# Kernel tuning notes

Hardware: AMD Instinct MI355X
Metric: run time of the kernel (lower is better)

## Reference

```python
import jax, jax.numpy as jnp
import numpy as np

B, N, H = 32, 2048, 256          # batch, num_docs, hidden_dim
F_HEADS = 8                      # config.dynamic_fusion_heads
NH = 8                           # num_heads inside each nn.MultiheadAttention
STEPS = 3                        # config.meta_adaptation_steps


def setup_inputs() -> dict:
    key = jax.random.key(0)
    ks = jax.random.split(key, 10)
    s = 0.02
    return {
        "query": jax.random.normal(ks[0], (B, H), jnp.float32),
        "retrieved_docs": jax.random.normal(ks[1], (B, N, H), jnp.float32),
        "causal_weights": jax.random.uniform(ks[2], (B, N, 1), jnp.float32),
        "context_history": jax.random.normal(ks[3], (B, H), jnp.float32),
        # per-fusion-head MultiheadAttention params (torch layout: in_proj [3H,H])
        "in_proj_w": jax.random.normal(ks[4], (F_HEADS, 3 * H, H), jnp.float32) * s,
        "in_proj_b": jnp.zeros((F_HEADS, 3 * H), jnp.float32),
        "out_proj_w": jax.random.normal(ks[5], (F_HEADS, H, H), jnp.float32) * s,
        "out_proj_b": jnp.zeros((F_HEADS, H), jnp.float32),
        "strategy_w": jax.random.normal(ks[6], (F_HEADS, H), jnp.float32) * s,
        "strategy_b": jnp.zeros((F_HEADS,), jnp.float32),
        "meta_params": jax.random.normal(ks[7], (STEPS, H, H), jnp.float32) * 0.02,
    }


def _mha_qlen1(q, kv, Wi, bi, Wo, bo):
    # q: [B,H] (query length 1), kv: [B,N,H]. Torch MHA semantics, batch_first.
    Wq, Wk, Wv = jnp.split(Wi, 3, axis=0)
    bq, bk, bv = jnp.split(bi, 3)
    dh = H // NH
    qh = (q @ Wq.T + bq).reshape(B, NH, dh)
    kh = (kv @ Wk.T + bk).reshape(B, N, NH, dh)
    vh = (kv @ Wv.T + bv).reshape(B, N, NH, dh)
    scores = jnp.einsum('bhd,bnhd->bhn', qh, kh) / jnp.sqrt(jnp.float32(dh))
    attn = jax.nn.softmax(scores, axis=-1)
    ctx = jnp.einsum('bhn,bnhd->bhd', attn, vh).reshape(B, H)
    return ctx @ Wo.T + bo


def reference(query, retrieved_docs, causal_weights, context_history,
              in_proj_w, in_proj_b, out_proj_w, out_proj_b,
              strategy_w, strategy_b, meta_params):
    # causal weighting of retrieved docs (shared across all fusion heads)
    weighted_docs = retrieved_docs * causal_weights  # [B,N,H]

    # batch all 8 fusion heads' cross-attention in one vmapped pass -> [F,B,H]
    heads_out = jax.vmap(
        lambda Wi, bi, Wo, bo: _mha_qlen1(query, weighted_docs, Wi, bi, Wo, bo)
    )(in_proj_w, in_proj_b, out_proj_w, out_proj_b)

    # sequential residual meta-adaptation steps (same matrices for every head)
    for i in range(STEPS):
        heads_out = heads_out + heads_out @ meta_params[i]

    # strategy-weighted combine of fusion heads
    strategy = jax.nn.softmax(query @ strategy_w.T + strategy_b, axis=-1)  # [B,F]
    return jnp.einsum('fbh,bf->bh', heads_out, strategy)  # [B,H]
```

## Files before the change

### kernel.cpp

```cpp
#include <hip/hip_runtime.h>
#include <hip/hip_bf16.h>


#define B_ 32
#define N_ 2048
#define H_ 256
#define F_ 8
#define FH_ 64
#define NCH_ 8

typedef unsigned short u16;
typedef __attribute__((ext_vector_type(8))) short bf16x8;
typedef __attribute__((ext_vector_type(4))) float f32x4;
#define MFMA(a, b, c) __builtin_amdgcn_mfma_f32_16x16x32_bf16((a), (b), (c), 0, 0, 0)

__device__ __forceinline__ u16 f2b(float x) {
  unsigned u = __builtin_bit_cast(unsigned, x);
  return (u16)((u + 0x7fffu + ((u >> 16) & 1u)) >> 16);
}
__device__ __forceinline__ float b2f(u16 h) {
  unsigned u = ((unsigned)h) << 16;
  return __builtin_bit_cast(float, u);
}
__device__ __forceinline__ bf16x8 ld8b(const float* p) {
  float4 v0 = *(const float4*)p, v1 = *(const float4*)(p + 4);
  bf16x8 a;
  a[0] = f2b(v0.x); a[1] = f2b(v0.y); a[2] = f2b(v0.z); a[3] = f2b(v0.w);
  a[4] = f2b(v1.x); a[5] = f2b(v1.y); a[6] = f2b(v1.z); a[7] = f2b(v1.w);
  return a;
}

static constexpr size_t UB_U     = 0;
static constexpr size_t UB_W     = 1048576;
static constexpr size_t UB_L     = 3145728;
static constexpr size_t UB_STRAT = 3153920;
static constexpr size_t UB_MT    = 3154944;

__global__ __launch_bounds__(512) void k1_fused(
    const float* __restrict__ query, const float* __restrict__ ipw,
    const float* __restrict__ ipb, const float* __restrict__ stw,
    const float* __restrict__ stb, const float* __restrict__ meta,
    u16* __restrict__ u, u16* __restrict__ metaT, float* __restrict__ strat)
{
  const int tid = threadIdx.x, L = tid & 63, w = tid >> 6;
  const int khi = L >> 4, col = L & 15;

  if (blockIdx.x >= 16) {
    const int bid2 = blockIdx.x - 16;
    const int s = bid2 >> 3, x0 = (bid2 & 7) * 32;
    __shared__ u16 sT[32 * 264];
    #pragma unroll
    for (int p = 0; p < 4; ++p) {
      int idx = tid + 512 * p;
      int r = idx >> 3, xq = (idx & 7) * 4;
      float4 v = *(const float4*)&meta[((size_t)(s * 256) + r) * 256 + x0 + xq];
      sT[(xq + 0) * 264 + r] = f2b(v.x);
      sT[(xq + 1) * 264 + r] = f2b(v.y);
      sT[(xq + 2) * 264 + r] = f2b(v.z);
      sT[(xq + 3) * 264 + r] = f2b(v.w);
    }
    __syncthreads();
    #pragma unroll
    for (int p = 0; p < 2; ++p) {
      int idx = tid + 512 * p;
      int x = idx >> 5, rq = (idx & 31) * 8;
      bf16x8 v = *(bf16x8*)&sT[x * 264 + rq];
      *(bf16x8*)&metaT[((size_t)(s * 256) + x0 + x) * 256 + rq] = v;
    }
    return;
  }

  const int f = blockIdx.x >> 1, hf = blockIdx.x & 1;
  __shared__ u16 sW[256 * 40];
  __shared__ u16 qhh[32 * 136];
  __shared__ u16 qhl[32 * 136];
  __shared__ float slog[256];

  bf16x8 qf[2][8];
  #pragma unroll
  for (int bt = 0; bt < 2; ++bt)
    #pragma unroll
    for (int ks = 0; ks < 8; ++ks)
      qf[bt][ks] = ld8b(&query[(size_t)(bt * 16 + col) * H_ + ks * 32 + khi * 8]);

  if (f == 0 && hf == 0 && w == 0) {
    f32x4 sacc[2] = {(f32x4){0.f,0.f,0.f,0.f}, (f32x4){0.f,0.f,0.f,0.f}};
    #pragma unroll
    for (int ks = 0; ks < 8; ++ks) {
      bf16x8 a = (bf16x8){0,0,0,0,0,0,0,0};
      if (col < 8) a = ld8b(&stw[(size_t)col * H_ + ks * 32 + khi * 8]);
      sacc[0] = MFMA(a, qf[0][ks], sacc[0]);
      sacc[1] = MFMA(a, qf[1][ks], sacc[1]);
    }
    if (khi < 2) {
      #pragma unroll
      for (int bt = 0; bt < 2; ++bt)
        #pragma unroll
        for (int r = 0; r < 4; ++r) {
          int i = khi * 4 + r;
          slog[(bt * 16 + col) * 8 + i] = sacc[bt][r] + stb[i];
        }
    }
  }

  f32x4 qacc[2] = {(f32x4){0.f,0.f,0.f,0.f}, (f32x4){0.f,0.f,0.f,0.f}};
  for (int ks = 0; ks < 8; ++ks) {
    #pragma unroll
    for (int p = 0; p < 2; ++p) {
      int gid = tid + 512 * p;
      int r = gid >> 3, kq = (gid & 7) * 4;
      float4 v = *(const float4*)&ipw[((size_t)(f * 768) + hf * 128 + r) * H_ + ks * 32 + kq];
      *(ushort4*)&sW[r * 40 + kq] = make_ushort4(f2b(v.x), f2b(v.y), f2b(v.z), f2b(v.w));
    }
    __syncthreads();
    bf16x8 a = *(const bf16x8*)&sW[(w * 16 + col) * 40 + khi * 8];
    qacc[0] = MFMA(a, qf[0][ks], qacc[0]);
    qacc[1] = MFMA(a, qf[1][ks], qacc[1]);
    __syncthreads();
  }
  {
    int r0 = w * 16 + khi * 4;
    float4 bq = *(const float4*)&ipb[f * 768 + hf * 128 + r0];
    #pragma unroll
    for (int bt = 0; bt < 2; ++bt) {
      int b = bt * 16 + col;
      float v0 = qacc[bt][0] + bq.x, v1 = qacc[bt][1] + bq.y;
      float v2 = qacc[bt][2] + bq.z, v3 = qacc[bt][3] + bq.w;
      ushort4 hs = make_ushort4(f2b(v0), f2b(v1), f2b(v2), f2b(v3));
      ushort4 ls = make_ushort4(f2b(v0 - b2f(hs.x)), f2b(v1 - b2f(hs.y)),
                                f2b(v2 - b2f(hs.z)), f2b(v3 - b2f(hs.w)));
      *(ushort4*)&qhh[b * 136 + r0] = hs;
      *(ushort4*)&qhl[b * 136 + r0] = ls;
    }
  }
  __syncthreads();

  if (f == 0 && hf == 0 && tid < 32) {
    float mx = slog[tid * 8];
    #pragma unroll
    for (int i = 1; i < F_; ++i) mx = fmaxf(mx, slog[tid * 8 + i]);
    float s = 0.f, e[F_];
    #pragma unroll
    for (int i = 0; i < F_; ++i) { e[i] = __expf(slog[tid * 8 + i] - mx); s += e[i]; }
    #pragma unroll
    for (int i = 0; i < F_; ++i) strat[tid * F_ + i] = e[i] / s;
  }

  const float scale = 0.17677669529663687f;
  for (int hh = 0; hh < 4; ++hh) {
    #pragma unroll
    for (int p = 0; p < 4; ++p) {
      int gid = tid + 512 * p;
      int d = gid >> 6, jq = (gid & 63) * 4;
      float4 v = *(const float4*)&ipw[((size_t)(f * 768 + 256) + (hf * 4 + hh) * 32 + d) * H_ + jq];
      float vv[4] = {v.x, v.y, v.z, v.w};
      #pragma unroll
      for (int e = 0; e < 4; ++e) {
        int j = jq + e;
        sW[j * 40 + (d ^ (((j >> 4) & 3) << 3))] = f2b(vv[e]);
      }
    }
    __syncthreads();
    #pragma unroll
    for (int q = 0; q < 2; ++q) {
      int jt = w * 2 + q;
      bf16x8 a = *(const bf16x8*)&sW[(jt * 16 + col) * 40 + ((khi ^ (jt & 3)) * 8)];
      #pragma unroll
      for (int bt = 0; bt < 2; ++bt) {
        int b = bt * 16 + col;
        bf16x8 bh = *(const bf16x8*)&qhh[b * 136 + hh * 32 + khi * 8];
        bf16x8 bl = *(const bf16x8*)&qhl[b * 136 + hh * 32 + khi * 8];
        f32x4 acc = (f32x4){0.f, 0.f, 0.f, 0.f};
        acc = MFMA(a, bh, acc);
        acc = MFMA(a, bl, acc);
        int j0 = jt * 16 + khi * 4;
        ushort4 us = make_ushort4(f2b(acc[0] * scale), f2b(acc[1] * scale),
                                  f2b(acc[2] * scale), f2b(acc[3] * scale));
        *(ushort4*)&u[((size_t)(b * 64) + f * 8 + hf * 4 + hh) * H_ + j0] = us;
      }
    }
    __syncthreads();
  }
}

__global__ __launch_bounds__(512) void k4_one(
    const float* __restrict__ docs, const float* __restrict__ cw,
    const u16* __restrict__ u, float* __restrict__ wbuf, float* __restrict__ lbuf)
{
  const int ns = blockIdx.x, b = blockIdx.y;
  const int n0 = ns * 256;
  const int tid = threadIdx.x, L = tid & 63, w = tid >> 6;
  const int khi = L >> 4, col = L & 15;
  const int ft = w & 3, nt0 = (w >> 2) * 2;

  __shared__ u16 sdu[64 * 264];
  __shared__ u16 phu[64 * 72];
  __shared__ u16 plou[64 * 72];

  bf16x8 uf[8];
  #pragma unroll
  for (int ks = 0; ks < 8; ++ks)
    uf[ks] = *(const bf16x8*)&u[((size_t)(b * 64) + ft * 16 + col) * H_ + ks * 32 + khi * 8];

  float4 dv[8];
  #pragma unroll
  for (int p = 0; p < 8; ++p) {
    int idx = tid + 512 * p;
    int n = idx >> 6, jq = (idx & 63) * 4;
    dv[p] = *(const float4*)&docs[((size_t)(b * N_) + n0 + n) * H_ + jq];
  }
  #pragma unroll
  for (int p = 0; p < 8; ++p) {
    int idx = tid + 512 * p;
    int n = idx >> 6, jq = (idx & 63) * 4;
    *(ushort4*)&sdu[n * 264 + (jq ^ (((n >> 3) & 3) << 4))] =
        make_ushort4(f2b(dv[p].x), f2b(dv[p].y), f2b(dv[p].z), f2b(dv[p].w));
  }
  __syncthreads();

  f32x4 acc2[4][2];
  #pragma unroll
  for (int mt = 0; mt < 4; ++mt)
    #pragma unroll
    for (int jt = 0; jt < 2; ++jt) acc2[mt][jt] = (f32x4){0.f, 0.f, 0.f, 0.f};
  float eacc[4] = {0.f, 0.f, 0.f, 0.f};

  for (int nc = 0; nc < 4; ++nc) {
    if (nc < 3) {
      #pragma unroll
      for (int p = 0; p < 8; ++p) {
        int idx = tid + 512 * p;
        int n = idx >> 6, jq = (idx & 63) * 4;
        dv[p] = *(const float4*)&docs[((size_t)(b * N_) + n0 + (nc + 1) * 64 + n) * H_ + jq];
      }
    }
    f32x4 sc0 = (f32x4){0.f, 0.f, 0.f, 0.f}, sc1 = sc0;
    const int nr0 = nt0 * 16 + col, nr1 = (nt0 + 1) * 16 + col;
    const int sw0 = ((nr0 >> 3) & 3) << 4, sw1 = ((nr1 >> 3) & 3) << 4;
    #pragma unroll
    for (int ks = 0; ks < 8; ++ks) {
      bf16x8 b0 = *(const bf16x8*)&sdu[nr0 * 264 + ((ks * 32 + khi * 8) ^ sw0)];
      bf16x8 b1 = *(const bf16x8*)&sdu[nr1 * 264 + ((ks * 32 + khi * 8) ^ sw1)];
      sc0 = MFMA(uf[ks], b0, sc0);
      sc1 = MFMA(uf[ks], b1, sc1);
    }
    {
      int ng = n0 + nc * 64 + nt0 * 16 + col;
      float cv0 = cw[(size_t)b * N_ + ng];
      float cv1 = cw[(size_t)b * N_ + ng + 16];
      #pragma unroll
      for (int r = 0; r < 4; ++r) {
        int fh = ft * 16 + khi * 4 + r;
        float ex0 = __expf(sc0[r] * cv0);
        float ex1 = __expf(sc1[r] * cv1);
        eacc[r] += ex0 + ex1;
        float p0 = ex0 * cv0, p1 = ex1 * cv1;
        u16 h0 = f2b(p0), h1 = f2b(p1);
        phu [fh * 72 + nt0 * 16 + col]       = h0;
        plou[fh * 72 + nt0 * 16 + col]       = f2b(p0 - b2f(h0));
        phu [fh * 72 + (nt0 + 1) * 16 + col] = h1;
        plou[fh * 72 + (nt0 + 1) * 16 + col] = f2b(p1 - b2f(h1));
      }
    }
    __syncthreads();

    #pragma unroll
    for (int kk = 0; kk < 2; ++kk) {
      #pragma unroll
      for (int jt = 0; jt < 2; ++jt) {
        int j = w * 32 + jt * 16 + col;
        bf16x8 bb;
        #pragma unroll
        for (int jj = 0; jj < 8; ++jj)
          bb[jj] = (short)sdu[(kk * 32 + khi * 8 + jj) * 264 + (j ^ (khi << 4))];
        #pragma unroll
        for (int mt = 0; mt < 4; ++mt) {
          bf16x8 ah = *(const bf16x8*)&phu [(mt * 16 + col) * 72 + kk * 32 + khi * 8];
          bf16x8 al = *(const bf16x8*)&plou[(mt * 16 + col) * 72 + kk * 32 + khi * 8];
          acc2[mt][jt] = MFMA(ah, bb, acc2[mt][jt]);
          acc2[mt][jt] = MFMA(al, bb, acc2[mt][jt]);
        }
      }
    }
    __syncthreads();

    if (nc < 3) {
      #pragma unroll
      for (int p = 0; p < 8; ++p) {
        int idx = tid + 512 * p;
        int n = idx >> 6, jq = (idx & 63) * 4;
        *(ushort4*)&sdu[n * 264 + (jq ^ (((n >> 3) & 3) << 4))] =
            make_ushort4(f2b(dv[p].x), f2b(dv[p].y), f2b(dv[p].z), f2b(dv[p].w));
      }
      __syncthreads();
    }
  }
  #pragma unroll
  for (int mt = 0; mt < 4; ++mt)
    #pragma unroll
    for (int jt = 0; jt < 2; ++jt)
      #pragma unroll
      for (int r = 0; r < 4; ++r) {
        int fh = mt * 16 + khi * 4 + r;
        int j = w * 32 + jt * 16 + col;
        atomicAdd(&wbuf[((size_t)(b * 64) + fh) * H_ + j], acc2[mt][jt][r]);
      }
  #pragma unroll
  for (int r = 0; r < 4; ++r) {
    float e = eacc[r];
    e += __shfl_xor(e, 1, 64);
    e += __shfl_xor(e, 2, 64);
    e += __shfl_xor(e, 4, 64);
    e += __shfl_xor(e, 8, 64);
    if (col == 0)
      atomicAdd(&lbuf[(size_t)(b * 64) + ft * 16 + khi * 4 + r], e);
  }
}

__global__ __launch_bounds__(512) void k5_mfma(
    const float* __restrict__ ipw, const float* __restrict__ ipb,
    const float* __restrict__ opw, const float* __restrict__ opb,
    const u16* __restrict__ metaT, const float* __restrict__ wbuf,
    const float* __restrict__ lbuf, const float* __restrict__ strat,
    float* __restrict__ out)
{
  const int f = blockIdx.x & 7, b0 = (blockIdx.x >> 3) * 16;
  const int tid = threadIdx.x, L = tid & 63, w = tid >> 6;
  const int khi = L >> 4, col = L & 15;

  __shared__ u16 XAh[16 * 264], XAl[16 * 264];
  __shared__ u16 XBh[16 * 264], XBl[16 * 264];

  bf16x8 av[2][8];
  #pragma unroll
  for (int mt = 0; mt < 2; ++mt)
    #pragma unroll
    for (int ks = 0; ks < 8; ++ks)
      av[mt][ks] = ld8b(&ipw[((size_t)(f * 768 + 512) + w * 32 + mt * 16 + col) * H_
                             + ks * 32 + khi * 8]);
  const size_t wrow = ((size_t)((b0 + col) * 64) + f * 8 + w) * H_;
  const float li = 1.f / lbuf[(size_t)((b0 + col) * 64) + f * 8 + w];
  f32x4 cacc0 = (f32x4){0.f, 0.f, 0.f, 0.f};
  f32x4 cacc1 = (f32x4){0.f, 0.f, 0.f, 0.f};
  #pragma unroll
  for (int ks = 0; ks < 8; ++ks) {
    const float* p = &wbuf[wrow + ks * 32 + khi * 8];
    float4 v0 = *(const float4*)p, v1 = *(const float4*)(p + 4);
    float vv[8] = {v0.x, v0.y, v0.z, v0.w, v1.x, v1.y, v1.z, v1.w};
    bf16x8 bh, bl;
    #pragma unroll
    for (int e = 0; e < 8; ++e) {
      float x = vv[e] * li;
      u16 h = f2b(x);
      bh[e] = (short)h;
      bl[e] = (short)f2b(x - b2f(h));
    }
    cacc0 = MFMA(av[0][ks], bh, cacc0); cacc0 = MFMA(av[0][ks], bl, cacc0);
    cacc1 = MFMA(av[1][ks], bh, cacc1); cacc1 = MFMA(av[1][ks], bl, cacc1);
  }
  #pragma unroll
  for (int mt = 0; mt < 2; ++mt) {
    f32x4 cv = mt ? cacc1 : cacc0;
    #pragma unroll
    for (int r = 0; r < 4; ++r) {
      int d = mt * 16 + khi * 4 + r;
      float vv = cv[r] + ipb[f * 768 + 512 + w * 32 + d];
      u16 hi = f2b(vv);
      XAh[col * 264 + w * 32 + d] = hi;
      XAl[col * 264 + w * 32 + d] = f2b(vv - b2f(hi));
    }
  }

  bf16x8 bw[2][8];
  #pragma unroll
  for (int q = 0; q < 2; ++q)
    #pragma unroll
    for (int ks = 0; ks < 8; ++ks)
      bw[q][ks] = ld8b(&opw[((size_t)(f * 256) + (w * 2 + q) * 16 + col) * H_
                            + ks * 32 + khi * 8]);
  __syncthreads();

  f32x4 hr0, hr1;
  {
    float bo0 = opb[f * 256 + (w * 2 + 0) * 16 + col];
    float bo1 = opb[f * 256 + (w * 2 + 1) * 16 + col];
    hr0 = (f32x4){bo0, bo0, bo0, bo0};
    hr1 = (f32x4){bo1, bo1, bo1, bo1};
  }
  #pragma unroll
  for (int ks = 0; ks < 8; ++ks) {
    bf16x8 ah = *(const bf16x8*)&XAh[col * 264 + ks * 32 + khi * 8];
    bf16x8 al = *(const bf16x8*)&XAl[col * 264 + ks * 32 + khi * 8];
    hr0 = MFMA(ah, bw[0][ks], hr0); hr0 = MFMA(al, bw[0][ks], hr0);
    hr1 = MFMA(ah, bw[1][ks], hr1); hr1 = MFMA(al, bw[1][ks], hr1);
  }

  auto spill = [&](u16* Oh, u16* Ol) {
    #pragma unroll
    for (int q = 0; q < 2; ++q) {
      f32x4 hv = q ? hr1 : hr0;
      int x = (w * 2 + q) * 16 + col;
      #pragma unroll
      for (int r = 0; r < 4; ++r) {
        u16 hi = f2b(hv[r]);
        Oh[(khi * 4 + r) * 264 + x] = hi;
        Ol[(khi * 4 + r) * 264 + x] = f2b(hv[r] - b2f(hi));
      }
    }
  };
  auto meta_mm = [&](const u16* Ah_, const u16* Al_, int s) {
    f32x4 n0 = hr0, n1 = hr1;
    #pragma unroll
    for (int ks = 0; ks < 8; ++ks) {
      bf16x8 ah = *(const bf16x8*)&Ah_[col * 264 + ks * 32 + khi * 8];
      bf16x8 al = *(const bf16x8*)&Al_[col * 264 + ks * 32 + khi * 8];
      const u16* mrow = &metaT[((size_t)(s * 256) + (w * 2) * 16 + col) * 256 + ks * 32 + khi * 8];
      bf16x8 m0 = *(const bf16x8*)mrow;
      bf16x8 m1 = *(const bf16x8*)(mrow + 16 * 256);
      n0 = MFMA(ah, m0, n0); n0 = MFMA(al, m0, n0);
      n1 = MFMA(ah, m1, n1); n1 = MFMA(al, m1, n1);
    }
    hr0 = n0; hr1 = n1;
  };

  spill(XBh, XBl);
  __syncthreads();
  meta_mm(XBh, XBl, 0);
  spill(XAh, XAl);
  __syncthreads();
  meta_mm(XAh, XAl, 1);
  spill(XBh, XBl);
  __syncthreads();
  meta_mm(XBh, XBl, 2);

  #pragma unroll
  for (int q = 0; q < 2; ++q) {
    f32x4 hv = q ? hr1 : hr0;
    int x = (w * 2 + q) * 16 + col;
    #pragma unroll
    for (int r = 0; r < 4; ++r) {
      int b = khi * 4 + r;
      float sv = strat[(b0 + b) * F_ + f];
      atomicAdd(&out[(size_t)(b0 + b) * H_ + x], sv * hv[r]);
    }
  }
}

extern "C" void kernel_launch(void* const* d_in, const int* in_sizes, int n_in,
                              void* d_out, int out_size, void* d_ws, size_t ws_size,
                              hipStream_t stream) {
  const float* query = (const float*)d_in[0];
  const float* docs  = (const float*)d_in[1];
  const float* cw    = (const float*)d_in[2];
  const float* ipw   = (const float*)d_in[4];
  const float* ipb   = (const float*)d_in[5];
  const float* opw   = (const float*)d_in[6];
  const float* opb   = (const float*)d_in[7];
  const float* stw   = (const float*)d_in[8];
  const float* stb   = (const float*)d_in[9];
  const float* meta  = (const float*)d_in[10];
  float* out = (float*)d_out;

  char* base = (char*)d_ws;
  u16*   u     = (u16*)(base + UB_U);
  float* wbuf  = (float*)(base + UB_W);
  float* lbuf  = (float*)(base + UB_L);
  float* strat = (float*)(base + UB_STRAT);
  u16*   metaT = (u16*)(base + UB_MT);

  hipMemsetAsync(out, 0, (size_t)B_ * H_ * sizeof(float), stream);
  hipMemsetAsync(base + UB_W, 0,
                 (size_t)(B_ * FH_ * H_ * sizeof(float) + B_ * FH_ * sizeof(float)),
                 stream);
  k1_fused<<<dim3(40), 512, 0, stream>>>(query, ipw, ipb, stw, stb, meta, u, metaT, strat);
  k4_one<<<dim3(NCH_, B_), 512, 0, stream>>>(docs, cw, u, wbuf, lbuf);
  k5_mfma<<<dim3(16), 512, 0, stream>>>(ipw, ipb, opw, opb, metaT, wbuf, lbuf, strat, out);
}
```

Before: 192.6 us.

## Fuse three kernels and memsets into one cooperative kernel with grid syncs

Merges the projection, meta-transpose, doc-attention and output kernels, plus the two memsets, into a single cooperative launch of 256 blocks that uses grid-wide syncs between phases. Zeroing of the accumulators is done by otherwise idle blocks in phase one. The Q projection now loads its weights straight into registers instead of staging them through shared memory with a barrier per k-step, and the K-fold step handles two heads per shared-memory fill with a wider swizzle. This removes launch and memset overhead at the cost of grid-sync latency and one larger shared-memory allocation per block, and falls back to separate launches if the cooperative launch fails.

Result: slower. 333.6 us (+73.3%).

```diff
diff --git a/kernel.cpp b/kernel.cpp
--- a/kernel.cpp
+++ b/kernel.cpp
@@ -1,5 +1,8 @@
 #include <hip/hip_runtime.h>
 #include <hip/hip_bf16.h>
+#include <hip/hip_cooperative_groups.h>
+
+namespace cg = cooperative_groups;
 
 
 #define B_ 32
@@ -36,45 +39,19 @@
 static constexpr size_t UB_STRAT = 3153920;
 static constexpr size_t UB_MT    = 3154944;
 
-__global__ __launch_bounds__(512) void k1_fused(
+#define SMEM_BYTES 55296
+
+__device__ __forceinline__ void dev_k1(char* smem, int f, int hf,
     const float* __restrict__ query, const float* __restrict__ ipw,
     const float* __restrict__ ipb, const float* __restrict__ stw,
-    const float* __restrict__ stb, const float* __restrict__ meta,
-    u16* __restrict__ u, u16* __restrict__ metaT, float* __restrict__ strat)
+    const float* __restrict__ stb, u16* __restrict__ u, float* __restrict__ strat)
 {
   const int tid = threadIdx.x, L = tid & 63, w = tid >> 6;
   const int khi = L >> 4, col = L & 15;
-
-  if (blockIdx.x >= 16) {
-    const int bid2 = blockIdx.x - 16;
-    const int s = bid2 >> 3, x0 = (bid2 & 7) * 32;
-    __shared__ u16 sT[32 * 264];
-    #pragma unroll
-    for (int p = 0; p < 4; ++p) {
-      int idx = tid + 512 * p;
-      int r = idx >> 3, xq = (idx & 7) * 4;
-      float4 v = *(const float4*)&meta[((size_t)(s * 256) + r) * 256 + x0 + xq];
-      sT[(xq + 0) * 264 + r] = f2b(v.x);
-      sT[(xq + 1) * 264 + r] = f2b(v.y);
-      sT[(xq + 2) * 264 + r] = f2b(v.z);
-      sT[(xq + 3) * 264 + r] = f2b(v.w);
-    }
-    __syncthreads();
-    #pragma unroll
-    for (int p = 0; p < 2; ++p) {
-      int idx = tid + 512 * p;
-      int x = idx >> 5, rq = (idx & 31) * 8;
-      bf16x8 v = *(bf16x8*)&sT[x * 264 + rq];
-      *(bf16x8*)&metaT[((size_t)(s * 256) + x0 + x) * 256 + rq] = v;
-    }
-    return;
-  }
-
-  const int f = blockIdx.x >> 1, hf = blockIdx.x & 1;
-  __shared__ u16 sW[256 * 40];
-  __shared__ u16 qhh[32 * 136];
-  __shared__ u16 qhl[32 * 136];
-  __shared__ float slog[256];
+  u16* sW2 = (u16*)smem;
+  u16* qhh = (u16*)(smem + 36864);
+  u16* qhl = (u16*)(smem + 45568);
+  float* slog = (float*)(smem + 54272);
 
   bf16x8 qf[2][8];
   #pragma unroll
@@ -103,20 +80,15 @@
     }
   }
 
+  bf16x8 aq[8];
+  #pragma unroll
+  for (int ks = 0; ks < 8; ++ks)
+    aq[ks] = ld8b(&ipw[((size_t)(f * 768) + hf * 128 + w * 16 + col) * H_ + ks * 32 + khi * 8]);
   f32x4 qacc[2] = {(f32x4){0.f,0.f,0.f,0.f}, (f32x4){0.f,0.f,0.f,0.f}};
+  #pragma unroll
   for (int ks = 0; ks < 8; ++ks) {
-    #pragma unroll
-    for (int p = 0; p < 2; ++p) {
-      int gid = tid + 512 * p;
-      int r = gid >> 3, kq = (gid & 7) * 4;
-      float4 v = *(const float4*)&ipw[((size_t)(f * 768) + hf * 128 + r) * H_ + ks * 32 + kq];
-      *(ushort4*)&sW[r * 40 + kq] = make_ushort4(f2b(v.x), f2b(v.y), f2b(v.z), f2b(v.w));
-    }
-    __syncthreads();
-    bf16x8 a = *(const bf16x8*)&sW[(w * 16 + col) * 40 + khi * 8];
-    qacc[0] = MFMA(a, qf[0][ks], qacc[0]);
-    qacc[1] = MFMA(a, qf[1][ks], qacc[1]);
-    __syncthreads();
+    qacc[0] = MFMA(aq[ks], qf[0][ks], qacc[0]);
+    qacc[1] = MFMA(aq[ks], qf[1][ks], qacc[1]);
   }
   {
     int r0 = w * 16 + khi * 4;
@@ -147,55 +119,87 @@
   }
 
   const float scale = 0.17677669529663687f;
-  for (int hh = 0; hh < 4; ++hh) {
-    #pragma unroll
-    for (int p = 0; p < 4; ++p) {
+  #pragma unroll
+  for (int hp = 0; hp < 2; ++hp) {
+    #pragma unroll
+    for (int p = 0; p < 8; ++p) {
       int gid = tid + 512 * p;
-      int d = gid >> 6, jq = (gid & 63) * 4;
-      float4 v = *(const float4*)&ipw[((size_t)(f * 768 + 256) + (hf * 4 + hh) * 32 + d) * H_ + jq];
+      int dr = gid >> 6, jq = (gid & 63) * 4;
+      float4 v = *(const float4*)&ipw[((size_t)(f * 768 + 256) + hf * 128 + hp * 64 + dr) * H_ + jq];
       float vv[4] = {v.x, v.y, v.z, v.w};
       #pragma unroll
-      for (int e = 0; e < 4; ++e) {
-        int j = jq + e;
-        sW[j * 40 + (d ^ (((j >> 4) & 3) << 3))] = f2b(vv[e]);
+      for (int e2 = 0; e2 < 4; ++e2) {
+        int j = jq + e2;
+        int m = ((((j >> 4) & 3) ^ ((j >> 2) & 3)) << 3);
+        sW2[j * 72 + (dr ^ m)] = f2b(vv[e2]);
       }
     }
     __syncthreads();
     #pragma unroll
-    for (int q = 0; q < 2; ++q) {
-      int jt = w * 2 + q;
-      bf16x8 a = *(const bf16x8*)&sW[(jt * 16 + col) * 40 + ((khi ^ (jt & 3)) * 8)];
-      #pragma unroll
-      for (int bt = 0; bt < 2; ++bt) {
-        int b = bt * 16 + col;
-        bf16x8 bh = *(const bf16x8*)&qhh[b * 136 + hh * 32 + khi * 8];
-        bf16x8 bl = *(const bf16x8*)&qhl[b * 136 + hh * 32 + khi * 8];
-        f32x4 acc = (f32x4){0.f, 0.f, 0.f, 0.f};
-        acc = MFMA(a, bh, acc);
-        acc = MFMA(a, bl, acc);
-        int j0 = jt * 16 + khi * 4;
-        ushort4 us = make_ushort4(f2b(acc[0] * scale), f2b(acc[1] * scale),
-                                  f2b(acc[2] * scale), f2b(acc[3] * scale));
-        *(ushort4*)&u[((size_t)(b * 64) + f * 8 + hf * 4 + hh) * H_ + j0] = us;
+    for (int e = 0; e < 2; ++e) {
+      #pragma unroll
+      for (int q = 0; q < 2; ++q) {
+        int jt = w * 2 + q;
+        bf16x8 a = *(const bf16x8*)&sW2[(jt * 16 + col) * 72 + e * 32
+                                        + ((khi ^ (jt & 3) ^ (col >> 2)) << 3)];
+        #pragma unroll
+        for (int bt = 0; bt < 2; ++bt) {
+          int b = bt * 16 + col;
+          int rl = (hp * 2 + e) * 32 + khi * 8;
+          bf16x8 bh = *(const bf16x8*)&qhh[b * 136 + rl];
+          bf16x8 bl = *(const bf16x8*)&qhl[b * 136 + rl];
+          f32x4 acc = (f32x4){0.f, 0.f, 0.f, 0.f};
+          acc = MFMA(a, bh, acc);
+          acc = MFMA(a, bl, acc);
+          int j0 = jt * 16 + khi * 4;
+          ushort4 us = make_ushort4(f2b(acc[0] * scale), f2b(acc[1] * scale),
+                                    f2b(acc[2] * scale), f2b(acc[3] * scale));
+          *(ushort4*)&u[((size_t)(b * 64) + f * 8 + hf * 4 + hp * 2 + e) * H_ + j0] = us;
+        }
       }
     }
     __syncthreads();
   }
 }
 
-__global__ __launch_bounds__(512) void k4_one(
+__device__ __forceinline__ void dev_meta(char* smem, int bid2,
+    const float* __restrict__ meta, u16* __restrict__ metaT)
+{
+  const int tid = threadIdx.x;
+  const int s = bid2 >> 3, x0 = (bid2 & 7) * 32;
+  u16* sT = (u16*)smem;
+  #pragma unroll
+  for (int p = 0; p < 4; ++p) {
+    int idx = tid + 512 * p;
+    int r = idx >> 3, xq = (idx & 7) * 4;
+    float4 v = *(const float4*)&meta[((size_t)(s * 256) + r) * 256 + x0 + xq];
+    sT[(xq + 0) * 264 + r] = f2b(v.x);
+    sT[(xq + 1) * 264 + r] = f2b(v.y);
+    sT[(xq + 2) * 264 + r] = f2b(v.z);
+    sT[(xq + 3) * 264 + r] = f2b(v.w);
+  }
+  __syncthreads();
+  #pragma unroll
+  for (int p = 0; p < 2; ++p) {
+    int idx = tid + 512 * p;
+    int x = idx >> 5, rq = (idx & 31) * 8;
+    bf16x8 v = *(bf16x8*)&sT[x * 264 + rq];
+    *(bf16x8*)&metaT[((size_t)(s * 256) + x0 + x) * 256 + rq] = v;
+  }
+}
+
+__device__ __forceinline__ void dev_k4(char* smem, int ns, int b,
     const float* __restrict__ docs, const float* __restrict__ cw,
     const u16* __restrict__ u, float* __restrict__ wbuf, float* __restrict__ lbuf)
 {
-  const int ns = blockIdx.x, b = blockIdx.y;
   const int n0 = ns * 256;
   const int tid = threadIdx.x, L = tid & 63, w = tid >> 6;
   const int khi = L >> 4, col = L & 15;
   const int ft = w & 3, nt0 = (w >> 2) * 2;
 
-  __shared__ u16 sdu[64 * 264];
-  __shared__ u16 phu[64 * 72];
-  __shared__ u16 plou[64 * 72];
+  u16* sdu  = (u16*)smem;
+  u16* phu  = (u16*)(smem + 33792);
+  u16* plou = (u16*)(smem + 43008);
 
   bf16x8 uf[8];
   #pragma unroll
@@ -317,19 +321,20 @@
   }
 }
 
-__global__ __launch_bounds__(512) void k5_mfma(
+__device__ __forceinline__ void dev_k5(char* smem, int f, int b0,
     const float* __restrict__ ipw, const float* __restrict__ ipb,
     const float* __restrict__ opw, const float* __restrict__ opb,
     const u16* __restrict__ metaT, const float* __restrict__ wbuf,
     const float* __restrict__ lbuf, const float* __restrict__ strat,
     float* __restrict__ out)
 {
-  const int f = blockIdx.x & 7, b0 = (blockIdx.x >> 3) * 16;
   const int tid = threadIdx.x, L = tid & 63, w = tid >> 6;
   const int khi = L >> 4, col = L & 15;
 
-  __shared__ u16 XAh[16 * 264], XAl[16 * 264];
-  __shared__ u16 XBh[16 * 264], XBl[16 * 264];
+  u16* XAh = (u16*)smem;
+  u16* XAl = (u16*)(smem + 8448);
+  u16* XBh = (u16*)(smem + 16896);
+  u16* XBl = (u16*)(smem + 25344);
 
   bf16x8 av[2][8];
   #pragma unroll
@@ -444,6 +449,75 @@
       atomicAdd(&out[(size_t)(b0 + b) * H_ + x], sv * hv[r]);
     }
   }
+}
+
+__global__ __launch_bounds__(512) void fused_all(
+    const float* __restrict__ query, const float* __restrict__ docs,
+    const float* __restrict__ cw, const float* __restrict__ ipw,
+    const float* __restrict__ ipb, const float* __restrict__ opw,
+    const float* __restrict__ opb, const float* __restrict__ stw,
+    const float* __restrict__ stb, const float* __restrict__ meta,
+    u16* __restrict__ u, u16* __restrict__ metaT, float* __restrict__ wbuf,
+    float* __restrict__ lbuf, float* __restrict__ strat, float* __restrict__ out)
+{
+  __shared__ __align__(16) char smem[SMEM_BYTES];
+  const int bid = blockIdx.x, tid = threadIdx.x;
+
+  if (bid < 16) {
+    dev_k1(smem, bid >> 1, bid & 1, query, ipw, ipb, stw, stb, u, strat);
+  } else if (bid < 40) {
+    dev_meta(smem, bid - 16, meta, metaT);
+  } else if (bid < 248) {
+    float4 z4 = make_float4(0.f, 0.f, 0.f, 0.f);
+    float4* z = (float4*)wbuf;
+    for (int i = (bid - 40) * 512 + tid; i < 131584; i += 208 * 512) z[i] = z4;
+  } else {
+    int i = (bid - 248) * 512 + tid;
+    out[i] = 0.f;
+    out[i + 4096] = 0.f;
+  }
+  __threadfence();
+  cg::this_grid().sync();
+
+  dev_k4(smem, bid & 7, bid >> 3, docs, cw, u, wbuf, lbuf);
+  __threadfence();
+  cg::this_grid().sync();
+
+  if (bid < 16)
+    dev_k5(smem, bid & 7, (bid >> 3) * 16, ipw, ipb, opw, opb, metaT, wbuf, lbuf, strat, out);
+}
+
+__global__ __launch_bounds__(512) void k1_sep(
+    const float* __restrict__ query, const float* __restrict__ ipw,
+    const float* __restrict__ ipb, const float* __restrict__ stw,
+    const float* __restrict__ stb, const float* __restrict__ meta,
+    u16* __restrict__ u, u16* __restrict__ metaT, float* __restrict__ strat)
+{
+  __shared__ __align__(16) char smem[SMEM_BYTES];
+  if (blockIdx.x < 16)
+    dev_k1(smem, blockIdx.x >> 1, blockIdx.x & 1, query, ipw, ipb, stw, stb, u, strat);
+  else
+    dev_meta(smem, blockIdx.x - 16, meta, metaT);
+}
+
+__global__ __launch_bounds__(512) void k4_sep(
+    const float* __restrict__ docs, const float* __restrict__ cw,
+    const u16* __restrict__ u, float* __restrict__ wbuf, float* __restrict__ lbuf)
+{
+  __shared__ __align__(16) char smem[SMEM_BYTES];
+  dev_k4(smem, blockIdx.x, blockIdx.y, docs, cw, u, wbuf, lbuf);
+}
+
+__global__ __launch_bounds__(512) void k5_sep(
+    const float* __restrict__ ipw, const float* __restrict__ ipb,
+    const float* __restrict__ opw, const float* __restrict__ opb,
+    const u16* __restrict__ metaT, const float* __restrict__ wbuf,
+    const float* __restrict__ lbuf, const float* __restrict__ strat,
+    float* __restrict__ out)
+{
+  __shared__ __align__(16) char smem[SMEM_BYTES];
+  dev_k5(smem, blockIdx.x & 7, (blockIdx.x >> 3) * 16,
+         ipw, ipb, opw, opb, metaT, wbuf, lbuf, strat, out);
 }
 
 extern "C" void kernel_launch(void* const* d_in, const int* in_sizes, int n_in,
@@ -468,11 +542,22 @@
   float* strat = (float*)(base + UB_STRAT);
   u16*   metaT = (u16*)(base + UB_MT);
 
-  hipMemsetAsync(out, 0, (size_t)B_ * H_ * sizeof(float), stream);
-  hipMemsetAsync(base + UB_W, 0,
-                 (size_t)(B_ * FH_ * H_ * sizeof(float) + B_ * FH_ * sizeof(float)),
-                 stream);
-  k1_fused<<<dim3(40), 512, 0, stream>>>(query, ipw, ipb, stw, stb, meta, u, metaT, strat);
-  k4_one<<<dim3(NCH_, B_), 512, 0, stream>>>(docs, cw, u, wbuf, lbuf);
-  k5_mfma<<<dim3(16), 512, 0, stream>>>(ipw, ipb, opw, opb, metaT, wbuf, lbuf, strat, out);
-}
+  void* args[16] = {
+    (void*)&query, (void*)&docs, (void*)&cw, (void*)&ipw, (void*)&ipb,
+    (void*)&opw, (void*)&opb, (void*)&stw, (void*)&stb, (void*)&meta,
+    (void*)&u, (void*)&metaT, (void*)&wbuf, (void*)&lbuf, (void*)&strat,
+    (void*)&out
+  };
+  hipError_t err = hipLaunchCooperativeKernel(
+      reinterpret_cast<void*>(fused_all), dim3(256), dim3(512), args, 0, stream);
+  if (err != hipSuccess) {
+    (void)hipGetLastError();
+    hipMemsetAsync(out, 0, (size_t)B_ * H_ * sizeof(float), stream);
+    hipMemsetAsync(base + UB_W, 0,
+                   (size_t)(B_ * FH_ * H_ * sizeof(float) + B_ * FH_ * sizeof(float)),
+                   stream);
+    k1_sep<<<dim3(40), 512, 0, stream>>>(query, ipw, ipb, stw, stb, meta, u, metaT, strat);
+    k4_sep<<<dim3(NCH_, B_), 512, 0, stream>>>(docs, cw, u, wbuf, lbuf);
+    k5_sep<<<dim3(16), 512, 0, stream>>>(ipw, ipb, opw, opb, metaT, wbuf, lbuf, strat, out);
+  }
+}
```
